# Kernel optimization log

Hardware: AMD Instinct MI355X
Metric: run time of the kernel (lower is better)

The kernel has to match this reference:

```python
import jax, jax.numpy as jnp
import numpy as np

B, L, D, H = 4, 8192, 512, 8


def _phi(x):
    # feature map: elu(x) + 1 (strictly positive)
    return jax.nn.elu(x) + 1.0


def setup_inputs() -> dict:
    key = jax.random.key(0)
    k1, k2, k3 = jax.random.split(key, 3)
    x = jax.random.normal(k1, (B, L, D), dtype=jnp.float32)
    w_qkv = jax.random.normal(k2, (D, 3 * D), dtype=jnp.float32) * 0.02
    b_qkv = jnp.zeros((3 * D,), dtype=jnp.float32)
    w_out = jax.random.normal(k3, (D, D), dtype=jnp.float32) * 0.02
    b_out = jnp.zeros((D,), dtype=jnp.float32)
    return {"x": x, "w_qkv": w_qkv, "b_qkv": b_qkv, "w_out": w_out,
            "b_out": b_out, "num_heads": H}


def reference(x, w_qkv, b_qkv, w_out, b_out, num_heads):
    Bx, Lx, Dx = x.shape
    dh = Dx // num_heads
    qkv = x @ w_qkv + b_qkv                       # (B, L, 3D)
    q, k, v = jnp.split(qkv, 3, axis=-1)
    # (B, L, D) -> (B, H, L, dh)
    def to_heads(t):
        return t.reshape(Bx, Lx, num_heads, dh).transpose(0, 2, 1, 3)
    q = _phi(to_heads(q))
    k = _phi(to_heads(k))
    v = to_heads(v)
    # kv[b,h,m,d] = sum_l k[b,h,l,d] * v[b,h,l,m]
    kv = jnp.einsum('bhld,bhlm->bhmd', k, v)      # (B, H, dh, dh)
    k_sum = jnp.sum(k, axis=2, keepdims=True)     # (B, H, 1, dh)
    # z[b,h,l,1] = 1 / <q_l, k_sum + 1e-6>
    z = 1.0 / jnp.einsum('bhld,bhmd->bhlm', q, k_sum + 1e-6)  # (B,H,L,1)
    out = jnp.einsum('bhld,bhmd->bhlm', q, kv) * z            # (B,H,L,dh)
    out = out.transpose(0, 2, 1, 3).reshape(Bx, Lx, Dx)
    return out @ w_out + b_out
```

## Files before the change

kernel.cpp:

```cpp
#include <hip/hip_runtime.h>
#include <hip/hip_bf16.h>
#include <math.h>

#define BB 4
#define LL 8192
#define DD 512
#define HH 8
#define MM (BB*LL)
#define NQKV 1536
#define CH 16

typedef __attribute__((ext_vector_type(4))) float f32x4;
typedef __attribute__((ext_vector_type(8))) short s16x8;
typedef __attribute__((ext_vector_type(4))) short s16x4;

__device__ __forceinline__ float bf2f(short u) {
  union { unsigned int i; float f; } c;
  c.i = ((unsigned int)(unsigned short)u) << 16;
  return c.f;
}
__device__ __forceinline__ short f2bf(float f) {
  union { float f; unsigned int i; } c; c.f = f;
  unsigned int r = c.i + 0x7FFFu + ((c.i >> 16) & 1u);
  return (short)(r >> 16);
}

__device__ __forceinline__ void gload16(const void* g, void* l) {
  __builtin_amdgcn_global_load_lds(
      (const __attribute__((address_space(1))) void*)(g),
      (__attribute__((address_space(3))) void*)(l), 16, 0, 0);
}

__global__ void conv_bf16(const float* __restrict__ in, short* __restrict__ out, int n) {
  int i = (blockIdx.x * blockDim.x + threadIdx.x) * 8;
  if (i < n) {
    float4 v0 = *reinterpret_cast<const float4*>(in + i);
    float4 v1 = *reinterpret_cast<const float4*>(in + i + 4);
    s16x8 o;
    o[0] = f2bf(v0.x); o[1] = f2bf(v0.y); o[2] = f2bf(v0.z); o[3] = f2bf(v0.w);
    o[4] = f2bf(v1.x); o[5] = f2bf(v1.y); o[6] = f2bf(v1.z); o[7] = f2bf(v1.w);
    *reinterpret_cast<s16x8*>(out + i) = o;
  }
}

__global__ void conv_wt(const float* __restrict__ w, short* __restrict__ wt, int K, int N) {
  int idx = blockIdx.x * blockDim.x + threadIdx.x;
  if (idx < K * N) {
    int n = idx / K, k = idx - n * K;
    wt[idx] = f2bf(w[(size_t)k * N + n]);
  }
}

template<int MODE>
__global__ __launch_bounds__(512, 4)
void gemm_bt(const short* __restrict__ A, const short* __restrict__ BT,
             const float* __restrict__ bias, void* __restrict__ Cout,
             short* __restrict__ ktb, short* __restrict__ vtb)
{
  constexpr int KD = 512;
  __shared__ __align__(16) char lds[65536];

  const int tid = threadIdx.x;
  const int wv = tid >> 6, lane = tid & 63;
  const int wm = wv >> 1, wn = wv & 1;
  const int fr = lane & 15, fq = lane >> 4;

  const int gx = gridDim.x;
  const int gy = gridDim.y;
  const int d = blockIdx.y * gx + blockIdx.x;
  const int nwg = gx * gy;
  const int lin = (d & 7) * (nwg >> 3) + (d >> 3);
  const int m0 = (lin / gy) * 256, n0 = (lin % gy) * 128;

  const int srow = tid >> 3;
  const int sunit = (tid & 7) ^ (srow & 7);
  const short* Ag = A  + (size_t)(m0 + srow) * KD + sunit * 8;
  const short* Bg = BT + (size_t)(n0 + srow) * KD + sunit * 8;
  char* ldsw = lds + wv * 1024;

  f32x4 acc[4][4] = {};

  for (int t = 0; t < 8; ++t) {
    const int k0 = t * 64;
#pragma unroll
    for (int i = 0; i < 4; ++i)
      gload16(Ag + (size_t)(i * 64) * KD + k0, ldsw + i * 8192);
#pragma unroll
    for (int i = 0; i < 2; ++i)
      gload16(Bg + (size_t)(i * 64) * KD + k0, ldsw + 32768 + i * 8192);
    __syncthreads();
#pragma unroll
    for (int kk = 0; kk < 2; ++kk) {
      s16x8 af[4], bfg[4];
#pragma unroll
      for (int i = 0; i < 4; ++i) {
        const int ra = wm * 64 + i * 16 + fr;
        const int ua = (kk * 4 + fq) ^ (ra & 7);
        af[i] = *(const s16x8*)(lds + ra * 128 + ua * 16);
      }
#pragma unroll
      for (int j = 0; j < 4; ++j) {
        const int rb = wn * 64 + j * 16 + fr;
        const int ub = (kk * 4 + fq) ^ (rb & 7);
        bfg[j] = *(const s16x8*)(lds + 32768 + rb * 128 + ub * 16);
      }
#pragma unroll
      for (int i = 0; i < 4; ++i)
#pragma unroll
        for (int j = 0; j < 4; ++j)
          acc[i][j] = __builtin_amdgcn_mfma_f32_16x16x32_bf16(af[i], bfg[j], acc[i][j], 0, 0, 0);
    }
    __syncthreads();
  }

  if (MODE == 0) {
    if (n0 < 512) {
      short* scr = (short*)lds;
#pragma unroll
      for (int j = 0; j < 4; ++j) {
        const int col = wn * 64 + j * 16 + fr;
        const float bv = bias[n0 + col];
#pragma unroll
        for (int i = 0; i < 4; ++i) {
          const int row = wm * 64 + i * 16 + fq * 4;
#pragma unroll
          for (int r = 0; r < 4; ++r) {
            float v = acc[i][j][r] + bv;
            v = (v > 0.f) ? (v + 1.f) : __expf(v);
            scr[(row + r) * 128 + col] = f2bf(v);
          }
        }
      }
      __syncthreads();
#pragma unroll
      for (int p = 0; p < 8; ++p) {
        const int off = p * 8192 + tid * 16;
        const int row = off >> 8, colb = off & 255;
        s16x8 v = *(const s16x8*)(lds + off);
        *(s16x8*)((short*)Cout + (size_t)(m0 + row) * 512 + n0 + (colb >> 1)) = v;
      }
    } else {
      const bool do_phi = (n0 < 1024);
      short* tdst = do_phi ? ktb : vtb;
      const int f0 = n0 - (do_phi ? 512 : 1024);
#pragma unroll
      for (int j = 0; j < 4; ++j) {
        const int col = wn * 64 + j * 16 + fr;
        const float bv = bias[n0 + col];
        const int cx = col & 31;
#pragma unroll
        for (int i = 0; i < 4; ++i) {
          const int l = wm * 64 + i * 16 + fq * 4;
          s16x4 pk;
#pragma unroll
          for (int r = 0; r < 4; ++r) {
            float v = acc[i][j][r] + bv;
            if (do_phi) v = (v > 0.f) ? (v + 1.f) : __expf(v);
            pk[r] = f2bf(v);
          }
          *(s16x4*)(lds + col * 512 + (((l >> 3) ^ cx) * 16) + (l & 7) * 2) = pk;
        }
      }
      __syncthreads();
#pragma unroll
      for (int p = 0; p < 8; ++p) {
        const int g = p * 512 + tid;
        const int col = g >> 5, up = g & 31;
        const int u = up ^ (col & 31);
        s16x8 v = *(const s16x8*)(lds + col * 512 + up * 16);
        const int f = f0 + col;
        const int hb = ((m0 >> 13) << 3) + (f >> 6);
        short* dst = tdst + ((size_t)hb * 64 + (f & 63)) * 8192 + (m0 & 8191) + u * 8;
        *(s16x8*)dst = v;
      }
    }
  } else {
    float* scrf = (float*)lds;
#pragma unroll
    for (int h = 0; h < 2; ++h) {
      __syncthreads();
      if ((wm >> 1) == h) {
#pragma unroll
        for (int j = 0; j < 4; ++j) {
          const int col = wn * 64 + j * 16 + fr;
          const float bv = bias[n0 + col];
#pragma unroll
          for (int i = 0; i < 4; ++i) {
            const int row = (wm & 1) * 64 + i * 16 + fq * 4;
#pragma unroll
            for (int r = 0; r < 4; ++r)
              scrf[(row + r) * 128 + col] = acc[i][j][r] + bv;
          }
        }
      }
      __syncthreads();
#pragma unroll
      for (int p = 0; p < 8; ++p) {
        const int off = p * 8192 + tid * 16;
        const int row = off >> 9, colb = off & 511;
        float4 v = *(const float4*)(lds + off);
        *(float4*)((float*)Cout + (size_t)(m0 + h * 128 + row) * 512 + n0 + (colb >> 2)) = v;
      }
    }
  }
}

__global__ __launch_bounds__(256, 4)
void kv_mfma(const short* __restrict__ kt, const short* __restrict__ vt,
             float* __restrict__ pkv, float* __restrict__ pks)
{
  const int hb = blockIdx.x, c = blockIdx.y;
  const int tid = threadIdx.x, wv = tid >> 6, lane = tid & 63;
  const int fr = lane & 15, fq = lane >> 4;
  const size_t base = (size_t)hb * 64 * 8192;
  const int l0 = c * 512;
  const short* vrow = vt + base + (size_t)fr * 8192 + l0 + fq * 8;
  const short* krow = kt + base + (size_t)(wv * 16 + fr) * 8192 + l0 + fq * 8;

  s16x8 ones;
#pragma unroll
  for (int j = 0; j < 8; ++j) ones[j] = (short)0x3F80;

  f32x4 acc[4] = {};
  f32x4 accd = {};
#pragma unroll
  for (int ks = 0; ks < 16; ++ks) {
    s16x8 bfr = *(const s16x8*)(krow + ks * 32);
    accd = __builtin_amdgcn_mfma_f32_16x16x32_bf16(ones, bfr, accd, 0, 0, 0);
#pragma unroll
    for (int i = 0; i < 4; ++i) {
      s16x8 af = *(const s16x8*)(vrow + (size_t)(i * 16) * 8192 + ks * 32);
      acc[i] = __builtin_amdgcn_mfma_f32_16x16x32_bf16(af, bfr, acc[i], 0, 0, 0);
    }
  }
  float* o = pkv + ((size_t)hb * CH + c) * 4096;
#pragma unroll
  for (int i = 0; i < 4; ++i)
#pragma unroll
    for (int r = 0; r < 4; ++r)
      o[(i * 16 + fq * 4 + r) * 64 + wv * 16 + fr] = acc[i][r];
  if (fq == 0)
    pks[((size_t)hb * CH + c) * 64 + wv * 16 + fr] = accd[0];
}

__global__ void kv_reduce(const float* __restrict__ pkv, const float* __restrict__ pks,
                          short* __restrict__ kv_b, short* __restrict__ ksum_b)
{
  const int idx = blockIdx.x * 256 + threadIdx.x;
  const int head = idx >> 12, md = idx & 4095;
  float s = 0.f;
  for (int i = 0; i < CH; ++i) s += pkv[((size_t)head * CH + i) * 4096 + md];
  kv_b[idx] = f2bf(s);
  if (md < 64) {
    float t = 0.f;
    for (int i = 0; i < CH; ++i) t += pks[((size_t)head * CH + i) * 64 + md];
    ksum_b[head * 64 + md] = f2bf(t + 1e-6f);
  }
}

__global__ __launch_bounds__(256, 2)
void attn_mfma(const short* __restrict__ q_b, const short* __restrict__ kv_b,
               const short* __restrict__ ksum_b, short* __restrict__ attn)
{
  const int hb = blockIdx.x;
  const int tile = blockIdx.y;
  const int b = hb >> 3, h = hb & 7;
  const int tid = threadIdx.x, wv = tid >> 6, lane = tid & 63;
  const int fr = lane & 15, fk = (lane >> 4) * 8;

  const short* kvp = kv_b + (size_t)hb * 4096;
  s16x8 bfrag[4][2];
#pragma unroll
  for (int j = 0; j < 4; ++j)
#pragma unroll
    for (int kk = 0; kk < 2; ++kk)
      bfrag[j][kk] = *(const s16x8*)(kvp + (j * 16 + fr) * 64 + kk * 32 + fk);
  s16x8 bden[2];
#pragma unroll
  for (int kk = 0; kk < 2; ++kk)
    bden[kk] = *(const s16x8*)(ksum_b + hb * 64 + kk * 32 + fk);

  const short* qb = q_b + (size_t)b * LL * DD + h * 64;
  const int l0 = tile * 256 + wv * 64;
  f32x4 accn[4][4] = {};
  f32x4 accd[4] = {};
#pragma unroll
  for (int i = 0; i < 4; ++i) {
#pragma unroll
    for (int kk = 0; kk < 2; ++kk) {
      s16x8 a = *(const s16x8*)(qb + (size_t)(l0 + i * 16 + fr) * DD + kk * 32 + fk);
      accd[i] = __builtin_amdgcn_mfma_f32_16x16x32_bf16(a, bden[kk], accd[i], 0, 0, 0);
#pragma unroll
      for (int j = 0; j < 4; ++j)
        accn[i][j] = __builtin_amdgcn_mfma_f32_16x16x32_bf16(a, bfrag[j][kk], accn[i][j], 0, 0, 0);
    }
  }

  short* ob = attn + (size_t)b * LL * DD + h * 64;
  const int fq = lane >> 4;
#pragma unroll
  for (int i = 0; i < 4; ++i) {
#pragma unroll
    for (int r = 0; r < 4; ++r) {
      const int row = l0 + i * 16 + fq * 4 + r;
      const float dinv = 1.0f / accd[i][r];
#pragma unroll
      for (int j = 0; j < 4; ++j) {
        ob[(size_t)row * DD + j * 16 + fr] = f2bf(accn[i][j][r] * dinv);
      }
    }
  }
}

extern "C" void kernel_launch(void* const* d_in, const int* in_sizes, int n_in,
                              void* d_out, int out_size, void* d_ws, size_t ws_size,
                              hipStream_t stream)
{
  const float* x     = (const float*)d_in[0];
  const float* w_qkv = (const float*)d_in[1];
  const float* b_qkv = (const float*)d_in[2];
  const float* w_out = (const float*)d_in[3];
  const float* b_out = (const float*)d_in[4];

  char* ws = (char*)d_ws;
  size_t off = 0;
  short* x_b   = (short*)(ws + off); off += (size_t)MM * DD * 2;
  short* wq_t  = (short*)(ws + off); off += (size_t)NQKV * DD * 2;
  short* wo_t  = (short*)(ws + off); off += (size_t)DD * DD * 2;
  short* q_b   = (short*)(ws + off); off += (size_t)MM * DD * 2;
  short* kt    = (short*)(ws + off); off += (size_t)32 * 64 * LL * 2;
  short* vt    = (short*)(ws + off); off += (size_t)32 * 64 * LL * 2;
  short* attn_b= (short*)(ws + off); off += (size_t)MM * DD * 2;
  float* pkv   = (float*)(ws + off); off += (size_t)32 * CH * 4096 * 4;
  float* pks   = (float*)(ws + off); off += (size_t)32 * CH * 64 * 4;
  short* kv_b  = (short*)(ws + off); off += (size_t)32 * 4096 * 2;
  short* ksum_b= (short*)(ws + off); off += (size_t)32 * 64 * 2;

  conv_bf16<<<dim3(MM * DD / 8 / 256), dim3(256), 0, stream>>>(x, x_b, MM * DD);
  conv_wt<<<dim3((DD * NQKV + 255) / 256), dim3(256), 0, stream>>>(w_qkv, wq_t, DD, NQKV);
  conv_wt<<<dim3((DD * DD + 255) / 256), dim3(256), 0, stream>>>(w_out, wo_t, DD, DD);

  gemm_bt<0><<<dim3(MM / 256, NQKV / 128), dim3(512), 0, stream>>>(
      x_b, wq_t, b_qkv, (void*)q_b, kt, vt);

  kv_mfma<<<dim3(32, CH), dim3(256), 0, stream>>>(kt, vt, pkv, pks);
  kv_reduce<<<dim3(512), dim3(256), 0, stream>>>(pkv, pks, kv_b, ksum_b);

  attn_mfma<<<dim3(32, 32), dim3(256), 0, stream>>>(q_b, kv_b, ksum_b, attn_b);

  gemm_bt<1><<<dim3(MM / 256, DD / 128), dim3(512), 0, stream>>>(
      attn_b, wo_t, b_out, d_out, nullptr, nullptr);
}
```

Measured before the change: 167.9 us.

## Fuse attention normalization with output projection GEMM in one kernel

Replaces the separate attention kernel and the output-projection GEMM with one fused kernel. Each 64-row block computes the normalized attention output per head into LDS, then multiplies it by the matching 64-row slice of the output weight, accumulating all 512 output columns. This removes the bf16 attention buffer's round trip through global memory and one kernel launch. In exchange it uses a smaller M tile (64 rows), so the W_out weight is reloaded per block, and the per-head loop is serialized with syncs that may limit MFMA throughput.

```diff
diff --git a/kernel.cpp b/kernel.cpp
--- a/kernel.cpp
+++ b/kernel.cpp
@@ -51,7 +51,6 @@
   }
 }
 
-template<int MODE>
 __global__ __launch_bounds__(512, 4)
 void gemm_bt(const short* __restrict__ A, const short* __restrict__ BT,
              const float* __restrict__ bias, void* __restrict__ Cout,
@@ -113,94 +112,64 @@
     __syncthreads();
   }
 
-  if (MODE == 0) {
-    if (n0 < 512) {
-      short* scr = (short*)lds;
-#pragma unroll
-      for (int j = 0; j < 4; ++j) {
-        const int col = wn * 64 + j * 16 + fr;
-        const float bv = bias[n0 + col];
-#pragma unroll
-        for (int i = 0; i < 4; ++i) {
-          const int row = wm * 64 + i * 16 + fq * 4;
-#pragma unroll
-          for (int r = 0; r < 4; ++r) {
-            float v = acc[i][j][r] + bv;
-            v = (v > 0.f) ? (v + 1.f) : __expf(v);
-            scr[(row + r) * 128 + col] = f2bf(v);
-          }
+  if (n0 < 512) {
+    short* scr = (short*)lds;
+#pragma unroll
+    for (int j = 0; j < 4; ++j) {
+      const int col = wn * 64 + j * 16 + fr;
+      const float bv = bias[n0 + col];
+#pragma unroll
+      for (int i = 0; i < 4; ++i) {
+        const int row = wm * 64 + i * 16 + fq * 4;
+#pragma unroll
+        for (int r = 0; r < 4; ++r) {
+          float v = acc[i][j][r] + bv;
+          v = (v > 0.f) ? (v + 1.f) : __expf(v);
+          scr[(row + r) * 128 + col] = f2bf(v);
         }
       }
-      __syncthreads();
-#pragma unroll
-      for (int p = 0; p < 8; ++p) {
-        const int off = p * 8192 + tid * 16;
-        const int row = off >> 8, colb = off & 255;
-        s16x8 v = *(const s16x8*)(lds + off);
-        *(s16x8*)((short*)Cout + (size_t)(m0 + row) * 512 + n0 + (colb >> 1)) = v;
-      }
-    } else {
-      const bool do_phi = (n0 < 1024);
-      short* tdst = do_phi ? ktb : vtb;
-      const int f0 = n0 - (do_phi ? 512 : 1024);
-#pragma unroll
-      for (int j = 0; j < 4; ++j) {
-        const int col = wn * 64 + j * 16 + fr;
-        const float bv = bias[n0 + col];
-        const int cx = col & 31;
-#pragma unroll
-        for (int i = 0; i < 4; ++i) {
-          const int l = wm * 64 + i * 16 + fq * 4;
-          s16x4 pk;
-#pragma unroll
-          for (int r = 0; r < 4; ++r) {
-            float v = acc[i][j][r] + bv;
-            if (do_phi) v = (v > 0.f) ? (v + 1.f) : __expf(v);
-            pk[r] = f2bf(v);
-          }
-          *(s16x4*)(lds + col * 512 + (((l >> 3) ^ cx) * 16) + (l & 7) * 2) = pk;
+    }
+    __syncthreads();
+#pragma unroll
+    for (int p = 0; p < 8; ++p) {
+      const int off = p * 8192 + tid * 16;
+      const int row = off >> 8, colb = off & 255;
+      s16x8 v = *(const s16x8*)(lds + off);
+      *(s16x8*)((short*)Cout + (size_t)(m0 + row) * 512 + n0 + (colb >> 1)) = v;
+    }
+  } else {
+    const bool do_phi = (n0 < 1024);
+    short* tdst = do_phi ? ktb : vtb;
+    const int f0 = n0 - (do_phi ? 512 : 1024);
+#pragma unroll
+    for (int j = 0; j < 4; ++j) {
+      const int col = wn * 64 + j * 16 + fr;
+      const float bv = bias[n0 + col];
+      const int cx = col & 31;
+#pragma unroll
+      for (int i = 0; i < 4; ++i) {
+        const int l = wm * 64 + i * 16 + fq * 4;
+        s16x4 pk;
+#pragma unroll
+        for (int r = 0; r < 4; ++r) {
+          float v = acc[i][j][r] + bv;
+          if (do_phi) v = (v > 0.f) ? (v + 1.f) : __expf(v);
+          pk[r] = f2bf(v);
         }
-      }
-      __syncthreads();
-#pragma unroll
-      for (int p = 0; p < 8; ++p) {
-        const int g = p * 512 + tid;
-        const int col = g >> 5, up = g & 31;
-        const int u = up ^ (col & 31);
-        s16x8 v = *(const s16x8*)(lds + col * 512 + up * 16);
-        const int f = f0 + col;
-        const int hb = ((m0 >> 13) << 3) + (f >> 6);
-        short* dst = tdst + ((size_t)hb * 64 + (f & 63)) * 8192 + (m0 & 8191) + u * 8;
-        *(s16x8*)dst = v;
-      }
-    }
-  } else {
-    float* scrf = (float*)lds;
-#pragma unroll
-    for (int h = 0; h < 2; ++h) {
-      __syncthreads();
-      if ((wm >> 1) == h) {
-#pragma unroll
-        for (int j = 0; j < 4; ++j) {
-          const int col = wn * 64 + j * 16 + fr;
-          const float bv = bias[n0 + col];
-#pragma unroll
-          for (int i = 0; i < 4; ++i) {
-            const int row = (wm & 1) * 64 + i * 16 + fq * 4;
-#pragma unroll
-            for (int r = 0; r < 4; ++r)
-              scrf[(row + r) * 128 + col] = acc[i][j][r] + bv;
-          }
-        }
-      }
-      __syncthreads();
-#pragma unroll
-      for (int p = 0; p < 8; ++p) {
-        const int off = p * 8192 + tid * 16;
-        const int row = off >> 9, colb = off & 511;
-        float4 v = *(const float4*)(lds + off);
-        *(float4*)((float*)Cout + (size_t)(m0 + h * 128 + row) * 512 + n0 + (colb >> 2)) = v;
-      }
+        *(s16x4*)(lds + col * 512 + (((l >> 3) ^ cx) * 16) + (l & 7) * 2) = pk;
+      }
+    }
+    __syncthreads();
+#pragma unroll
+    for (int p = 0; p < 8; ++p) {
+      const int g = p * 512 + tid;
+      const int col = g >> 5, up = g & 31;
+      const int u = up ^ (col & 31);
+      s16x8 v = *(const s16x8*)(lds + col * 512 + up * 16);
+      const int f = f0 + col;
+      const int hb = ((m0 >> 13) << 3) + (f >> 6);
+      short* dst = tdst + ((size_t)hb * 64 + (f & 63)) * 8192 + (m0 & 8191) + u * 8;
+      *(s16x8*)dst = v;
     }
   }
 }
@@ -259,56 +228,107 @@
 }
 
 __global__ __launch_bounds__(256, 2)
-void attn_mfma(const short* __restrict__ q_b, const short* __restrict__ kv_b,
-               const short* __restrict__ ksum_b, short* __restrict__ attn)
-{
-  const int hb = blockIdx.x;
-  const int tile = blockIdx.y;
-  const int b = hb >> 3, h = hb & 7;
-  const int tid = threadIdx.x, wv = tid >> 6, lane = tid & 63;
-  const int fr = lane & 15, fk = (lane >> 4) * 8;
-
-  const short* kvp = kv_b + (size_t)hb * 4096;
-  s16x8 bfrag[4][2];
-#pragma unroll
-  for (int j = 0; j < 4; ++j)
-#pragma unroll
-    for (int kk = 0; kk < 2; ++kk)
-      bfrag[j][kk] = *(const s16x8*)(kvp + (j * 16 + fr) * 64 + kk * 32 + fk);
-  s16x8 bden[2];
-#pragma unroll
-  for (int kk = 0; kk < 2; ++kk)
-    bden[kk] = *(const s16x8*)(ksum_b + hb * 64 + kk * 32 + fk);
-
-  const short* qb = q_b + (size_t)b * LL * DD + h * 64;
-  const int l0 = tile * 256 + wv * 64;
-  f32x4 accn[4][4] = {};
-  f32x4 accd[4] = {};
-#pragma unroll
-  for (int i = 0; i < 4; ++i) {
+void attn_out(const short* __restrict__ q_b, const short* __restrict__ kv_b,
+              const short* __restrict__ ksum_b, const short* __restrict__ wo_t,
+              const float* __restrict__ b_out, float* __restrict__ out)
+{
+  __shared__ __align__(16) char lds[73728];
+  const int tid = threadIdx.x;
+  const int wv = tid >> 6, lane = tid & 63;
+  const int fr = lane & 15, fq = lane >> 4;
+  const int l0 = blockIdx.x * 64;
+  const int bb = l0 >> 13;
+
+  const int srow = tid >> 3;
+  const int sunit = (tid & 7) ^ (srow & 7);
+  const short* Wg = wo_t + (size_t)srow * 512 + sunit * 8;
+  char* ldsw = lds + 8192 + wv * 1024;
+
+  f32x4 acc[4][8] = {};
+
+  for (int h = 0; h < 8; ++h) {
+#pragma unroll
+    for (int i = 0; i < 16; ++i)
+      gload16(Wg + (size_t)(i * 32) * 512 + h * 64, ldsw + i * 4096);
+
+    {
+      const int hb = bb * 8 + h;
+      const short* kvp = kv_b + (size_t)hb * 4096;
+      const short* ksp = ksum_b + hb * 64;
+      const short* qb = q_b + (size_t)(l0 + wv * 16) * 512 + h * 64;
+      f32x4 accn[4] = {};
+      f32x4 accd = {};
+#pragma unroll
+      for (int kk = 0; kk < 2; ++kk) {
+        s16x8 a = *(const s16x8*)(qb + (size_t)fr * 512 + kk * 32 + fq * 8);
+        s16x8 bden = *(const s16x8*)(ksp + kk * 32 + fq * 8);
+        accd = __builtin_amdgcn_mfma_f32_16x16x32_bf16(a, bden, accd, 0, 0, 0);
+#pragma unroll
+        for (int j = 0; j < 4; ++j) {
+          s16x8 bfr = *(const s16x8*)(kvp + (j * 16 + fr) * 64 + kk * 32 + fq * 8);
+          accn[j] = __builtin_amdgcn_mfma_f32_16x16x32_bf16(a, bfr, accn[j], 0, 0, 0);
+        }
+      }
+#pragma unroll
+      for (int r = 0; r < 4; ++r) {
+        const int row = wv * 16 + fq * 4 + r;
+        const float dinv = 1.0f / accd[r];
+#pragma unroll
+        for (int j = 0; j < 4; ++j) {
+          const int col = j * 16 + fr;
+          *(short*)(lds + row * 128 + (((col >> 3) ^ (row & 7)) << 4) + ((col & 7) << 1))
+              = f2bf(accn[j][r] * dinv);
+        }
+      }
+    }
+    __syncthreads();
+
 #pragma unroll
     for (int kk = 0; kk < 2; ++kk) {
-      s16x8 a = *(const s16x8*)(qb + (size_t)(l0 + i * 16 + fr) * DD + kk * 32 + fk);
-      accd[i] = __builtin_amdgcn_mfma_f32_16x16x32_bf16(a, bden[kk], accd[i], 0, 0, 0);
-#pragma unroll
-      for (int j = 0; j < 4; ++j)
-        accn[i][j] = __builtin_amdgcn_mfma_f32_16x16x32_bf16(a, bfrag[j][kk], accn[i][j], 0, 0, 0);
-    }
-  }
-
-  short* ob = attn + (size_t)b * LL * DD + h * 64;
-  const int fq = lane >> 4;
-#pragma unroll
-  for (int i = 0; i < 4; ++i) {
-#pragma unroll
-    for (int r = 0; r < 4; ++r) {
-      const int row = l0 + i * 16 + fq * 4 + r;
-      const float dinv = 1.0f / accd[i][r];
-#pragma unroll
-      for (int j = 0; j < 4; ++j) {
-        ob[(size_t)row * DD + j * 16 + fr] = f2bf(accn[i][j][r] * dinv);
-      }
-    }
+      s16x8 af[4];
+#pragma unroll
+      for (int i = 0; i < 4; ++i) {
+        const int row = i * 16 + fr;
+        const int u = (kk * 4 + fq) ^ (row & 7);
+        af[i] = *(const s16x8*)(lds + row * 128 + u * 16);
+      }
+#pragma unroll
+      for (int j = 0; j < 8; ++j) {
+        const int n = wv * 128 + j * 16 + fr;
+        const int u = (kk * 4 + fq) ^ (n & 7);
+        s16x8 bw = *(const s16x8*)(lds + 8192 + n * 128 + u * 16);
+#pragma unroll
+        for (int i = 0; i < 4; ++i)
+          acc[i][j] = __builtin_amdgcn_mfma_f32_16x16x32_bf16(af[i], bw, acc[i][j], 0, 0, 0);
+      }
+    }
+    __syncthreads();
+  }
+
+  float* scrf = (float*)lds;
+#pragma unroll
+  for (int p = 0; p < 2; ++p) {
+#pragma unroll
+    for (int ii = 0; ii < 2; ++ii) {
+      const int i = 2 * p + ii;
+#pragma unroll
+      for (int j = 0; j < 8; ++j) {
+        const int col = wv * 128 + j * 16 + fr;
+        const float bv = b_out[col];
+#pragma unroll
+        for (int r = 0; r < 4; ++r)
+          scrf[(ii * 16 + fq * 4 + r) * 512 + col] = acc[i][j][r] + bv;
+      }
+    }
+    __syncthreads();
+#pragma unroll
+    for (int pp = 0; pp < 16; ++pp) {
+      const int off = pp * 4096 + tid * 16;
+      const int row = off >> 11, colb = off & 2047;
+      float4 v = *(const float4*)(lds + off);
+      *(float4*)(out + (size_t)(l0 + p * 32 + row) * 512 + (colb >> 2)) = v;
+    }
+    __syncthreads();
   }
 }
 
@@ -330,7 +350,6 @@
   short* q_b   = (short*)(ws + off); off += (size_t)MM * DD * 2;
   short* kt    = (short*)(ws + off); off += (size_t)32 * 64 * LL * 2;
   short* vt    = (short*)(ws + off); off += (size_t)32 * 64 * LL * 2;
-  short* attn_b= (short*)(ws + off); off += (size_t)MM * DD * 2;
   float* pkv   = (float*)(ws + off); off += (size_t)32 * CH * 4096 * 4;
   float* pks   = (float*)(ws + off); off += (size_t)32 * CH * 64 * 4;
   short* kv_b  = (short*)(ws + off); off += (size_t)32 * 4096 * 2;
@@ -340,14 +359,12 @@
   conv_wt<<<dim3((DD * NQKV + 255) / 256), dim3(256), 0, stream>>>(w_qkv, wq_t, DD, NQKV);
   conv_wt<<<dim3((DD * DD + 255) / 256), dim3(256), 0, stream>>>(w_out, wo_t, DD, DD);
 
-  gemm_bt<0><<<dim3(MM / 256, NQKV / 128), dim3(512), 0, stream>>>(
+  gemm_bt<<<dim3(MM / 256, NQKV / 128), dim3(512), 0, stream>>>(
       x_b, wq_t, b_qkv, (void*)q_b, kt, vt);
 
   kv_mfma<<<dim3(32, CH), dim3(256), 0, stream>>>(kt, vt, pkv, pks);
   kv_reduce<<<dim3(512), dim3(256), 0, stream>>>(pkv, pks, kv_b, ksum_b);
 
-  attn_mfma<<<dim3(32, 32), dim3(256), 0, stream>>>(q_b, kv_b, ksum_b, attn_b);
-
-  gemm_bt<1><<<dim3(MM / 256, DD / 128), dim3(512), 0, stream>>>(
-      attn_b, wo_t, b_out, d_out, nullptr, nullptr);
-}
+  attn_out<<<dim3(MM / 64), dim3(256), 0, stream>>>(
+      q_b, kv_b, ksum_b, wo_t, b_out, (float*)d_out);
+}
```

Measured after the change: 164.9 us (median of 2 runs). About the same (-1.8%).
